# Performance work log

Measured on AMD Instinct MI355X. Metric: run time of the kernel, lower is better.

The kernel has to match this reference:

```python
import jax, jax.numpy as jnp
import numpy as np

NUM_EDGES = 800_000
NUM_VERTICES = 100_000
NNZ = 1_600_000
D_MODEL = 128


def setup_inputs() -> dict:
    key = jax.random.key(0)
    ks = jax.random.split(key, 10)
    d = D_MODEL
    return {
        "x_e": jax.random.normal(ks[0], (NUM_EDGES, d), dtype=jnp.float32),
        "h_v": jax.random.normal(ks[1], (NUM_VERTICES, d), dtype=jnp.float32),
        "c_v": jax.random.normal(ks[2], (NUM_VERTICES, d), dtype=jnp.float32),
        "W_ih": jax.random.normal(ks[3], (4 * d, d), dtype=jnp.float32) * 0.05,
        "W_hh": jax.random.normal(ks[4], (4 * d, d), dtype=jnp.float32) * 0.05,
        "b_ih": jax.random.normal(ks[5], (4 * d,), dtype=jnp.float32) * 0.05,
        "b_hh": jax.random.normal(ks[6], (4 * d,), dtype=jnp.float32) * 0.05,
        "nnz_edge_ids": jax.random.randint(ks[7], (NNZ,), 0, NUM_EDGES, dtype=jnp.int32),
        "nnz_vertex_ids": jax.random.randint(ks[8], (NNZ,), 0, NUM_VERTICES, dtype=jnp.int32),
        "v_batch": jax.random.randint(ks[9], (NUM_VERTICES,), 0, 8, dtype=jnp.int32),
    }


def reference(x_e, h_v, c_v, W_ih, W_hh, b_ih, b_hh, nnz_edge_ids, nnz_vertex_ids, v_batch):
    # msg = adj_t.T @ x_e : scatter-add edge embeddings into incident vertices
    msg = jax.ops.segment_sum(x_e[nnz_edge_ids], nnz_vertex_ids,
                              num_segments=h_v.shape[0])  # [V, d]
    # single-step LSTM update (PyTorch gate order: i, f, g, o)
    gates = msg @ W_ih.T + b_ih + h_v @ W_hh.T + b_hh  # [V, 4d]
    i, f, g, o = jnp.split(gates, 4, axis=-1)
    i = jax.nn.sigmoid(i)
    f = jax.nn.sigmoid(f)
    g = jnp.tanh(g)
    o = jax.nn.sigmoid(o)
    c_new = f * c_v + i * g
    h_new = o * jnp.tanh(c_new)
    return (h_new, c_new)
```

## Files before the change

kernel.cpp:

```cpp
#include <hip/hip_runtime.h>
#include <hip/hip_bf16.h>

#define NE 800000
#define NV 100000
#define NNZN 1600000
#define D 128
#define SLOT_CAP 64
#define SC_BLOCKS 8192

typedef short short8 __attribute__((ext_vector_type(8)));
typedef short s16x4 __attribute__((ext_vector_type(4)));
typedef float f32x4 __attribute__((ext_vector_type(4)));
typedef float f32x8 __attribute__((ext_vector_type(8)));
typedef _Float16 h8v __attribute__((ext_vector_type(8)));

__device__ __forceinline__ unsigned short f2bfu(float f) {
  union { float f; unsigned u; } x;
  x.f = f;
  unsigned u = x.u;
  u += ((u >> 16) & 1u) + 0x7FFFu;
  return (unsigned short)(u >> 16);
}

__device__ __forceinline__ float fsigmoid(float x) {
  return 1.0f / (1.0f + __expf(-x));
}
__device__ __forceinline__ float ftanh(float x) {
  return 2.0f / (1.0f + __expf(-2.0f * x)) - 1.0f;
}

__device__ __forceinline__ f32x8 h2f8(h8v h) {
  f32x8 r;
#pragma unroll
  for (int k = 0; k < 8; ++k) r[k] = (float)h[k];
  return r;
}

__global__ __launch_bounds__(256) void wconv_kernel(
    const float* __restrict__ W_ih, const float* __restrict__ W_hh,
    const float* __restrict__ b_ih, const float* __restrict__ b_hh,
    short* __restrict__ Wcat, float* __restrict__ bcomb,
    int* __restrict__ counts) {
  int idx = blockIdx.x * 256 + threadIdx.x;
  if (idx < 16384) {
    int c8 = idx;
    int pos = c8 & 63;
    int t   = (c8 >> 6) & 1;
    int g   = (c8 >> 7) & 3;
    int kk  = (c8 >> 9) & 7;
    int wid = (c8 >> 12) & 3;
    int n = g * 128 + wid * 32 + t * 16 + (pos >> 2);
    int k0 = kk * 32 + (pos & 3) * 8;
    const float* src = (k0 < 128) ? (W_ih + (size_t)n * 128 + k0)
                                  : (W_hh + (size_t)n * 128 + (k0 - 128));
    f32x4 a = *(const f32x4*)(src);
    f32x4 b = *(const f32x4*)(src + 4);
    short8 v;
    v[0] = (short)f2bfu(a[0]); v[1] = (short)f2bfu(a[1]);
    v[2] = (short)f2bfu(a[2]); v[3] = (short)f2bfu(a[3]);
    v[4] = (short)f2bfu(b[0]); v[5] = (short)f2bfu(b[1]);
    v[6] = (short)f2bfu(b[2]); v[7] = (short)f2bfu(b[3]);
    *(short8*)(Wcat + (size_t)c8 * 8) = v;
  }
  if (idx < 512) bcomb[idx] = b_ih[idx] + b_hh[idx];
  if (idx < NV) counts[idx] = 0;
}

__global__ __launch_bounds__(256) void scatcon_kernel(
    const int* __restrict__ eid, const int* __restrict__ vid,
    int* __restrict__ counts, int* __restrict__ slots,
    const float* __restrict__ x_e, _Float16* __restrict__ x_h) {
  unsigned j = blockIdx.x * 256 + threadIdx.x;
  if (j < NNZN) {
    int v = vid[j];
    int pos = atomicAdd(&counts[v], 1);
    if (pos < SLOT_CAP) slots[(size_t)v * SLOT_CAP + pos] = eid[j];
  }
  const unsigned NU = (unsigned)NE * 16u;
  for (unsigned u = j; u < NU; u += SC_BLOCKS * 256u) {
    f32x4 a = __builtin_nontemporal_load((const f32x4*)(x_e + (size_t)u * 8));
    f32x4 b = __builtin_nontemporal_load((const f32x4*)(x_e + (size_t)u * 8 + 4));
    h8v h;
    h[0] = (_Float16)a[0]; h[1] = (_Float16)a[1];
    h[2] = (_Float16)a[2]; h[3] = (_Float16)a[3];
    h[4] = (_Float16)b[0]; h[5] = (_Float16)b[1];
    h[6] = (_Float16)b[2]; h[7] = (_Float16)b[3];
    *(h8v*)(x_h + (size_t)u * 8) = h;
  }
}

__global__ __launch_bounds__(256) void scatter_direct_kernel(
    const int* __restrict__ eid, const int* __restrict__ vid,
    int* __restrict__ counts, int* __restrict__ slots) {
  int j = blockIdx.x * 256 + threadIdx.x;
  if (j < NNZN) {
    int v = vid[j];
    int pos = atomicAdd(&counts[v], 1);
    if (pos < SLOT_CAP) slots[(size_t)v * SLOT_CAP + pos] = eid[j];
  }
}

__global__ __launch_bounds__(256, 4) void gather16_kernel(
    const _Float16* __restrict__ x_h, const int* __restrict__ counts,
    const int* __restrict__ slots, char* __restrict__ msgb) {
  __shared__ int slds[4][SLOT_CAP];
  const int tid = threadIdx.x;
  const int wid = tid >> 6;
  const int lane = tid & 63;
  const int v = blockIdx.x * 4 + wid;
  const int grp = lane >> 4;
  const int p16 = lane & 15;
  int deg = counts[v];
  deg = deg > SLOT_CAP ? SLOT_CAP : deg;
  slds[wid][lane] = slots[(size_t)v * SLOT_CAP + lane];
  const int* row_ids = slds[wid];

  f32x8 A0 = {0.f,0.f,0.f,0.f,0.f,0.f,0.f,0.f};
  f32x8 A1 = A0, A2 = A0, A3 = A0;
  const f32x8 Z = A0;
  const int nfull = deg >> 5;
  const int rem = deg & 31;
#pragma unroll 1
  for (int c = 0; c < nfull; ++c) {
    int b = c * 32 + grp;
    int e0 = row_ids[b];      int e1 = row_ids[b + 4];
    int e2 = row_ids[b + 8];  int e3 = row_ids[b + 12];
    int e4 = row_ids[b + 16]; int e5 = row_ids[b + 20];
    int e6 = row_ids[b + 24]; int e7 = row_ids[b + 28];
    h8v t0 = *(const h8v*)(x_h + (size_t)e0 * D + p16 * 8);
    h8v t1 = *(const h8v*)(x_h + (size_t)e1 * D + p16 * 8);
    h8v t2 = *(const h8v*)(x_h + (size_t)e2 * D + p16 * 8);
    h8v t3 = *(const h8v*)(x_h + (size_t)e3 * D + p16 * 8);
    h8v t4 = *(const h8v*)(x_h + (size_t)e4 * D + p16 * 8);
    h8v t5 = *(const h8v*)(x_h + (size_t)e5 * D + p16 * 8);
    h8v t6 = *(const h8v*)(x_h + (size_t)e6 * D + p16 * 8);
    h8v t7 = *(const h8v*)(x_h + (size_t)e7 * D + p16 * 8);
    A0 += h2f8(t0); A1 += h2f8(t1); A2 += h2f8(t2); A3 += h2f8(t3);
    A0 += h2f8(t4); A1 += h2f8(t5); A2 += h2f8(t6); A3 += h2f8(t7);
  }
  if (rem) {
    int b = nfull * 32 + grp;
    int i0 = b,      i1 = b + 4,  i2 = b + 8,  i3 = b + 12;
    int i4 = b + 16, i5 = b + 20, i6 = b + 24, i7 = b + 28;
    int e0 = row_ids[i0 < deg ? i0 : 0];
    int e1 = row_ids[i1 < deg ? i1 : 0];
    int e2 = row_ids[i2 < deg ? i2 : 0];
    int e3 = row_ids[i3 < deg ? i3 : 0];
    int e4 = row_ids[i4 < deg ? i4 : 0];
    int e5 = row_ids[i5 < deg ? i5 : 0];
    int e6 = row_ids[i6 < deg ? i6 : 0];
    int e7 = row_ids[i7 < deg ? i7 : 0];
    h8v t0 = *(const h8v*)(x_h + (size_t)e0 * D + p16 * 8);
    h8v t1 = *(const h8v*)(x_h + (size_t)e1 * D + p16 * 8);
    h8v t2 = *(const h8v*)(x_h + (size_t)e2 * D + p16 * 8);
    h8v t3 = *(const h8v*)(x_h + (size_t)e3 * D + p16 * 8);
    h8v t4 = *(const h8v*)(x_h + (size_t)e4 * D + p16 * 8);
    h8v t5 = *(const h8v*)(x_h + (size_t)e5 * D + p16 * 8);
    h8v t6 = *(const h8v*)(x_h + (size_t)e6 * D + p16 * 8);
    h8v t7 = *(const h8v*)(x_h + (size_t)e7 * D + p16 * 8);
    A0 += (i0 < deg) ? h2f8(t0) : Z;
    A1 += (i1 < deg) ? h2f8(t1) : Z;
    A2 += (i2 < deg) ? h2f8(t2) : Z;
    A3 += (i3 < deg) ? h2f8(t3) : Z;
    A0 += (i4 < deg) ? h2f8(t4) : Z;
    A1 += (i5 < deg) ? h2f8(t5) : Z;
    A2 += (i6 < deg) ? h2f8(t6) : Z;
    A3 += (i7 < deg) ? h2f8(t7) : Z;
  }
  A0 += A1;
  A2 += A3;
  A0 += A2;
#pragma unroll
  for (int f = 0; f < 8; ++f) {
    float x = A0[f];
    x += __shfl_xor(x, 32);
    x += __shfl_xor(x, 16);
    A0[f] = x;
  }
  if (lane < 16) {
    short8 p;
#pragma unroll
    for (int f = 0; f < 8; ++f) p[f] = (short)f2bfu(A0[f]);
    *(short8*)(msgb + (size_t)v * 512 + p16 * 16) = p;
  }
}

__global__ __launch_bounds__(256, 4) void gather_kernel(
    const float* __restrict__ x_e, const int* __restrict__ counts,
    const int* __restrict__ slots, char* __restrict__ msgb) {
  __shared__ int slds[4][SLOT_CAP];
  const int tid = threadIdx.x;
  const int wid = tid >> 6;
  const int lane = tid & 63;
  const int v = blockIdx.x * 4 + wid;
  const int half = lane >> 5;
  const int pos = lane & 31;
  int deg = counts[v];
  deg = deg > SLOT_CAP ? SLOT_CAP : deg;
  slds[wid][lane] = slots[(size_t)v * SLOT_CAP + lane];
  const int* row_ids = slds[wid];

  f32x4 a0 = {0.f, 0.f, 0.f, 0.f}, a1 = a0, a2 = a0, a3 = a0;
  const int nfull = deg >> 4;
  const int rem = deg & 15;
#pragma unroll 1
  for (int c = 0; c < nfull; ++c) {
    int b = c * 16 + half;
    int e0 = row_ids[b];      int e1 = row_ids[b + 2];
    int e2 = row_ids[b + 4];  int e3 = row_ids[b + 6];
    int e4 = row_ids[b + 8];  int e5 = row_ids[b + 10];
    int e6 = row_ids[b + 12]; int e7 = row_ids[b + 14];
    a0 += *(const f32x4*)(x_e + (size_t)e0 * D + pos * 4);
    a1 += *(const f32x4*)(x_e + (size_t)e1 * D + pos * 4);
    a2 += *(const f32x4*)(x_e + (size_t)e2 * D + pos * 4);
    a3 += *(const f32x4*)(x_e + (size_t)e3 * D + pos * 4);
    a0 += *(const f32x4*)(x_e + (size_t)e4 * D + pos * 4);
    a1 += *(const f32x4*)(x_e + (size_t)e5 * D + pos * 4);
    a2 += *(const f32x4*)(x_e + (size_t)e6 * D + pos * 4);
    a3 += *(const f32x4*)(x_e + (size_t)e7 * D + pos * 4);
  }
  if (rem) {
    int b = nfull * 16 + half;
    f32x4 z = {0.f, 0.f, 0.f, 0.f};
    int i0 = b,      i1 = b + 2,  i2 = b + 4,  i3 = b + 6;
    int i4 = b + 8,  i5 = b + 10, i6 = b + 12, i7 = b + 14;
    int e0 = row_ids[i0 < deg ? i0 : 0];
    int e1 = row_ids[i1 < deg ? i1 : 0];
    int e2 = row_ids[i2 < deg ? i2 : 0];
    int e3 = row_ids[i3 < deg ? i3 : 0];
    int e4 = row_ids[i4 < deg ? i4 : 0];
    int e5 = row_ids[i5 < deg ? i5 : 0];
    int e6 = row_ids[i6 < deg ? i6 : 0];
    int e7 = row_ids[i7 < deg ? i7 : 0];
    f32x4 t0 = *(const f32x4*)(x_e + (size_t)e0 * D + pos * 4);
    f32x4 t1 = *(const f32x4*)(x_e + (size_t)e1 * D + pos * 4);
    f32x4 t2 = *(const f32x4*)(x_e + (size_t)e2 * D + pos * 4);
    f32x4 t3 = *(const f32x4*)(x_e + (size_t)e3 * D + pos * 4);
    f32x4 t4 = *(const f32x4*)(x_e + (size_t)e4 * D + pos * 4);
    f32x4 t5 = *(const f32x4*)(x_e + (size_t)e5 * D + pos * 4);
    f32x4 t6 = *(const f32x4*)(x_e + (size_t)e6 * D + pos * 4);
    f32x4 t7 = *(const f32x4*)(x_e + (size_t)e7 * D + pos * 4);
    a0 += (i0 < deg) ? t0 : z;
    a1 += (i1 < deg) ? t1 : z;
    a2 += (i2 < deg) ? t2 : z;
    a3 += (i3 < deg) ? t3 : z;
    a0 += (i4 < deg) ? t4 : z;
    a1 += (i5 < deg) ? t5 : z;
    a2 += (i6 < deg) ? t6 : z;
    a3 += (i7 < deg) ? t7 : z;
  }
  a0 += a1;
  a2 += a3;
  a0 += a2;
  f32x4 b;
  b[0] = __shfl_xor(a0[0], 32);
  b[1] = __shfl_xor(a0[1], 32);
  b[2] = __shfl_xor(a0[2], 32);
  b[3] = __shfl_xor(a0[3], 32);
  a0 += b;
  if (half == 0) {
    s16x4 p;
    p[0] = (short)f2bfu(a0[0]);
    p[1] = (short)f2bfu(a0[1]);
    p[2] = (short)f2bfu(a0[2]);
    p[3] = (short)f2bfu(a0[3]);
    *(s16x4*)(msgb + (size_t)v * 512 + pos * 8) = p;
  }
}

__global__ __launch_bounds__(256) void lstm_kernel(
    const char* __restrict__ msgb, const float* __restrict__ h_v,
    const float* __restrict__ c_v, const short* __restrict__ Wcat,
    const float* __restrict__ bcomb, float* __restrict__ out) {
  __shared__ char Atile[32 * 256 * 2];
  const int tid = threadIdx.x;
  const int vbase = blockIdx.x * 32;

#pragma unroll
  for (int i = 0; i < 4; ++i) {
    int cid = tid + i * 256;
    int row = cid >> 5;
    int c = cid & 31;
    short8 v;
    if (c < 16) {
      v = *(const short8*)(msgb + (size_t)(vbase + row) * 512 + c * 16);
    } else {
      const float* src = h_v + (size_t)(vbase + row) * D + (c - 16) * 8;
      f32x4 a = *(const f32x4*)(src);
      f32x4 b = *(const f32x4*)(src + 4);
      v[0] = (short)f2bfu(a[0]); v[1] = (short)f2bfu(a[1]);
      v[2] = (short)f2bfu(a[2]); v[3] = (short)f2bfu(a[3]);
      v[4] = (short)f2bfu(b[0]); v[5] = (short)f2bfu(b[1]);
      v[6] = (short)f2bfu(b[2]); v[7] = (short)f2bfu(b[3]);
    }
    int byteoff = (row * 512 + c * 16) ^ ((row & 7) << 4);
    *(short8*)(Atile + byteoff) = v;
  }
  __syncthreads();

  const int wid = tid >> 6;
  const int lane = tid & 63;
  const int l16 = lane & 15;
  const int lhi = lane >> 4;

  f32x4 acc[2][4][2] = {};

#pragma unroll
  for (int kk = 0; kk < 8; ++kk) {
    short8 afrag[2];
#pragma unroll
    for (int m = 0; m < 2; ++m) {
      int row = m * 16 + l16;
      int byteoff = (row * 512 + kk * 64 + lhi * 16) ^ ((row & 7) << 4);
      afrag[m] = *(const short8*)(Atile + byteoff);
    }
#pragma unroll
    for (int g = 0; g < 4; ++g) {
#pragma unroll
      for (int t = 0; t < 2; ++t) {
        size_t boff = (size_t)(wid * 64 + kk * 8 + g * 2 + t) * 1024
                    + (size_t)(l16 * 4 + lhi) * 16;
        short8 bfrag = *(const short8*)((const char*)Wcat + boff);
        acc[0][g][t] = __builtin_amdgcn_mfma_f32_16x16x32_bf16(afrag[0], bfrag, acc[0][g][t], 0, 0, 0);
        acc[1][g][t] = __builtin_amdgcn_mfma_f32_16x16x32_bf16(afrag[1], bfrag, acc[1][g][t], 0, 0, 0);
      }
    }
  }

  float* out_h = out;
  float* out_c = out + (size_t)NV * D;
#pragma unroll
  for (int m = 0; m < 2; ++m) {
#pragma unroll
    for (int t = 0; t < 2; ++t) {
      int d = wid * 32 + t * 16 + l16;
      float bi = bcomb[d];
      float bf = bcomb[128 + d];
      float bg = bcomb[256 + d];
      float bo = bcomb[384 + d];
#pragma unroll
      for (int r = 0; r < 4; ++r) {
        int v = vbase + m * 16 + lhi * 4 + r;
        float gi = acc[m][0][t][r] + bi;
        float gf = acc[m][1][t][r] + bf;
        float gg = acc[m][2][t][r] + bg;
        float go = acc[m][3][t][r] + bo;
        float ii = fsigmoid(gi);
        float ff = fsigmoid(gf);
        float g_ = ftanh(gg);
        float oo = fsigmoid(go);
        float cv = c_v[(size_t)v * D + d];
        float cn = ff * cv + ii * g_;
        float hn = oo * ftanh(cn);
        out_h[(size_t)v * D + d] = hn;
        out_c[(size_t)v * D + d] = cn;
      }
    }
  }
}

extern "C" void kernel_launch(void* const* d_in, const int* in_sizes, int n_in,
                              void* d_out, int out_size, void* d_ws, size_t ws_size,
                              hipStream_t stream) {
  const float* x_e  = (const float*)d_in[0];
  const float* h_v  = (const float*)d_in[1];
  const float* c_v  = (const float*)d_in[2];
  const float* W_ih = (const float*)d_in[3];
  const float* W_hh = (const float*)d_in[4];
  const float* b_ih = (const float*)d_in[5];
  const float* b_hh = (const float*)d_in[6];
  const int* eid    = (const int*)d_in[7];
  const int* vid    = (const int*)d_in[8];
  float* out = (float*)d_out;

  char* w = (char*)d_ws;
  short* Wcat  = (short*)w;                 w += 512 * 256 * sizeof(short);
  float* bcomb = (float*)w;                 w += 512 * sizeof(float);
  int* counts  = (int*)w;                   w += NV * sizeof(int);
  int* slots   = (int*)w;                   w += (size_t)NV * SLOT_CAP * sizeof(int);
  _Float16* x_h = (_Float16*)w;

  const size_t need = 512 * 256 * sizeof(short) + 512 * sizeof(float)
                    + (size_t)NV * sizeof(int)
                    + (size_t)NV * SLOT_CAP * sizeof(int)
                    + (size_t)NE * D * sizeof(_Float16);

  char* msgb = (char*)(out + (size_t)NV * D);

  wconv_kernel<<<512, 256, 0, stream>>>(W_ih, W_hh, b_ih, b_hh, Wcat, bcomb, counts);
  if (ws_size >= need) {
    scatcon_kernel<<<SC_BLOCKS, 256, 0, stream>>>(eid, vid, counts, slots, x_e, x_h);
    gather16_kernel<<<NV / 4, 256, 0, stream>>>(x_h, counts, slots, msgb);
  } else {
    scatter_direct_kernel<<<(NNZN + 255) / 256, 256, 0, stream>>>(eid, vid, counts, slots);
    gather_kernel<<<NV / 4, 256, 0, stream>>>(x_e, counts, slots, msgb);
  }
  lstm_kernel<<<NV / 32, 256, 0, stream>>>(msgb, h_v, c_v, Wcat, bcomb, out);
}
```

Baseline: 419.1 us.

## Convert part of edge embeddings to fp16 in output buffer and workspace, gather mixed

The scatter pass now converts only edges below a cutoff to fp16. The first 400k rows go into the output buffer, which is free until the LSTM step, and further rows go into any spare workspace. The gather kernel reads fp16 rows for low edge ids and fp32 rows straight from x_e for the rest, using a second per-vertex counter. The second list of edge ids is stored from the back of each vertex's slot array. The message buffer moves into the workspace. The aim is to get most of the halved gather traffic when the workspace cannot hold a full fp16 copy, at the cost of conversion traffic and branchier gather code.

```diff
diff --git a/kernel.cpp b/kernel.cpp
--- a/kernel.cpp
+++ b/kernel.cpp
@@ -6,6 +6,7 @@
 #define NNZN 1600000
 #define D 128
 #define SLOT_CAP 64
+#define XCUT 400000
 #define SC_BLOCKS 8192
 
 typedef short short8 __attribute__((ext_vector_type(8)));
@@ -40,7 +41,7 @@
     const float* __restrict__ W_ih, const float* __restrict__ W_hh,
     const float* __restrict__ b_ih, const float* __restrict__ b_hh,
     short* __restrict__ Wcat, float* __restrict__ bcomb,
-    int* __restrict__ counts) {
+    int* __restrict__ counts, int* __restrict__ counts2) {
   int idx = blockIdx.x * 256 + threadIdx.x;
   if (idx < 16384) {
     int c8 = idx;
@@ -63,21 +64,30 @@
     *(short8*)(Wcat + (size_t)c8 * 8) = v;
   }
   if (idx < 512) bcomb[idx] = b_ih[idx] + b_hh[idx];
-  if (idx < NV) counts[idx] = 0;
+  if (idx < NV) { counts[idx] = 0; counts2[idx] = 0; }
 }
 
 __global__ __launch_bounds__(256) void scatcon_kernel(
     const int* __restrict__ eid, const int* __restrict__ vid,
-    int* __restrict__ counts, int* __restrict__ slots,
-    const float* __restrict__ x_e, _Float16* __restrict__ x_h) {
+    int* __restrict__ counts, int* __restrict__ counts2,
+    int* __restrict__ slots, const float* __restrict__ x_e,
+    _Float16* __restrict__ xh0, _Float16* __restrict__ xh1, int ecut) {
   unsigned j = blockIdx.x * 256 + threadIdx.x;
   if (j < NNZN) {
     int v = vid[j];
-    int pos = atomicAdd(&counts[v], 1);
-    if (pos < SLOT_CAP) slots[(size_t)v * SLOT_CAP + pos] = eid[j];
-  }
-  const unsigned NU = (unsigned)NE * 16u;
+    int e = eid[j];
+    if (e < ecut) {
+      int pos = atomicAdd(&counts[v], 1);
+      if (pos < SLOT_CAP) slots[(size_t)v * SLOT_CAP + pos] = e;
+    } else {
+      int pos = atomicAdd(&counts2[v], 1);
+      if (pos < SLOT_CAP) slots[(size_t)v * SLOT_CAP + (SLOT_CAP - 1 - pos)] = e;
+    }
+  }
+  const unsigned NU = (unsigned)ecut * 16u;
   for (unsigned u = j; u < NU; u += SC_BLOCKS * 256u) {
+    unsigned row = u >> 4;
+    unsigned c8 = u & 15u;
     f32x4 a = __builtin_nontemporal_load((const f32x4*)(x_e + (size_t)u * 8));
     f32x4 b = __builtin_nontemporal_load((const f32x4*)(x_e + (size_t)u * 8 + 4));
     h8v h;
@@ -85,7 +95,9 @@
     h[2] = (_Float16)a[2]; h[3] = (_Float16)a[3];
     h[4] = (_Float16)b[0]; h[5] = (_Float16)b[1];
     h[6] = (_Float16)b[2]; h[7] = (_Float16)b[3];
-    *(h8v*)(x_h + (size_t)u * 8) = h;
+    _Float16* dst = (row < XCUT) ? (xh0 + (size_t)row * D)
+                                 : (xh1 + (size_t)(row - XCUT) * D);
+    *(h8v*)(dst + c8 * 8) = h;
   }
 }
 
@@ -100,9 +112,11 @@
   }
 }
 
-__global__ __launch_bounds__(256, 4) void gather16_kernel(
-    const _Float16* __restrict__ x_h, const int* __restrict__ counts,
-    const int* __restrict__ slots, char* __restrict__ msgb) {
+__global__ __launch_bounds__(256, 4) void gather_mixed_kernel(
+    const float* __restrict__ x_e, const _Float16* __restrict__ xh0,
+    const _Float16* __restrict__ xh1, const int* __restrict__ counts,
+    const int* __restrict__ counts2, const int* __restrict__ slots,
+    unsigned short* __restrict__ msgws) {
   __shared__ int slds[4][SLOT_CAP];
   const int tid = threadIdx.x;
   const int wid = tid >> 6;
@@ -110,63 +124,90 @@
   const int v = blockIdx.x * 4 + wid;
   const int grp = lane >> 4;
   const int p16 = lane & 15;
-  int deg = counts[v];
-  deg = deg > SLOT_CAP ? SLOT_CAP : deg;
+  int degf = counts[v];   degf = degf > SLOT_CAP ? SLOT_CAP : degf;
+  int degb = counts2[v];  degb = degb > SLOT_CAP ? SLOT_CAP : degb;
   slds[wid][lane] = slots[(size_t)v * SLOT_CAP + lane];
   const int* row_ids = slds[wid];
 
   f32x8 A0 = {0.f,0.f,0.f,0.f,0.f,0.f,0.f,0.f};
   f32x8 A1 = A0, A2 = A0, A3 = A0;
   const f32x8 Z = A0;
-  const int nfull = deg >> 5;
-  const int rem = deg & 31;
+
+  const int nfull = degf >> 5;
+  const int rem = degf & 31;
 #pragma unroll 1
   for (int c = 0; c < nfull; ++c) {
     int b = c * 32 + grp;
-    int e0 = row_ids[b];      int e1 = row_ids[b + 4];
-    int e2 = row_ids[b + 8];  int e3 = row_ids[b + 12];
-    int e4 = row_ids[b + 16]; int e5 = row_ids[b + 20];
-    int e6 = row_ids[b + 24]; int e7 = row_ids[b + 28];
-    h8v t0 = *(const h8v*)(x_h + (size_t)e0 * D + p16 * 8);
-    h8v t1 = *(const h8v*)(x_h + (size_t)e1 * D + p16 * 8);
-    h8v t2 = *(const h8v*)(x_h + (size_t)e2 * D + p16 * 8);
-    h8v t3 = *(const h8v*)(x_h + (size_t)e3 * D + p16 * 8);
-    h8v t4 = *(const h8v*)(x_h + (size_t)e4 * D + p16 * 8);
-    h8v t5 = *(const h8v*)(x_h + (size_t)e5 * D + p16 * 8);
-    h8v t6 = *(const h8v*)(x_h + (size_t)e6 * D + p16 * 8);
-    h8v t7 = *(const h8v*)(x_h + (size_t)e7 * D + p16 * 8);
+    h8v t0, t1, t2, t3, t4, t5, t6, t7;
+#pragma unroll
+    for (int k = 0; k < 8; ++k) {
+      int e = row_ids[b + 4 * k];
+      const _Float16* p = (e < XCUT) ? (xh0 + (size_t)e * D)
+                                     : (xh1 + (size_t)(e - XCUT) * D);
+      h8v t = *(const h8v*)(p + p16 * 8);
+      switch (k) {
+        case 0: t0 = t; break; case 1: t1 = t; break;
+        case 2: t2 = t; break; case 3: t3 = t; break;
+        case 4: t4 = t; break; case 5: t5 = t; break;
+        case 6: t6 = t; break; case 7: t7 = t; break;
+      }
+    }
     A0 += h2f8(t0); A1 += h2f8(t1); A2 += h2f8(t2); A3 += h2f8(t3);
     A0 += h2f8(t4); A1 += h2f8(t5); A2 += h2f8(t6); A3 += h2f8(t7);
   }
   if (rem) {
     int b = nfull * 32 + grp;
-    int i0 = b,      i1 = b + 4,  i2 = b + 8,  i3 = b + 12;
-    int i4 = b + 16, i5 = b + 20, i6 = b + 24, i7 = b + 28;
-    int e0 = row_ids[i0 < deg ? i0 : 0];
-    int e1 = row_ids[i1 < deg ? i1 : 0];
-    int e2 = row_ids[i2 < deg ? i2 : 0];
-    int e3 = row_ids[i3 < deg ? i3 : 0];
-    int e4 = row_ids[i4 < deg ? i4 : 0];
-    int e5 = row_ids[i5 < deg ? i5 : 0];
-    int e6 = row_ids[i6 < deg ? i6 : 0];
-    int e7 = row_ids[i7 < deg ? i7 : 0];
-    h8v t0 = *(const h8v*)(x_h + (size_t)e0 * D + p16 * 8);
-    h8v t1 = *(const h8v*)(x_h + (size_t)e1 * D + p16 * 8);
-    h8v t2 = *(const h8v*)(x_h + (size_t)e2 * D + p16 * 8);
-    h8v t3 = *(const h8v*)(x_h + (size_t)e3 * D + p16 * 8);
-    h8v t4 = *(const h8v*)(x_h + (size_t)e4 * D + p16 * 8);
-    h8v t5 = *(const h8v*)(x_h + (size_t)e5 * D + p16 * 8);
-    h8v t6 = *(const h8v*)(x_h + (size_t)e6 * D + p16 * 8);
-    h8v t7 = *(const h8v*)(x_h + (size_t)e7 * D + p16 * 8);
-    A0 += (i0 < deg) ? h2f8(t0) : Z;
-    A1 += (i1 < deg) ? h2f8(t1) : Z;
-    A2 += (i2 < deg) ? h2f8(t2) : Z;
-    A3 += (i3 < deg) ? h2f8(t3) : Z;
-    A0 += (i4 < deg) ? h2f8(t4) : Z;
-    A1 += (i5 < deg) ? h2f8(t5) : Z;
-    A2 += (i6 < deg) ? h2f8(t6) : Z;
-    A3 += (i7 < deg) ? h2f8(t7) : Z;
-  }
+    h8v t[8];
+    int valid[8];
+#pragma unroll
+    for (int k = 0; k < 8; ++k) {
+      int i = b + 4 * k;
+      valid[k] = (i < degf);
+      int e = row_ids[valid[k] ? i : 0];
+      const _Float16* p = (e < XCUT) ? (xh0 + (size_t)e * D)
+                                     : (xh1 + (size_t)(e - XCUT) * D);
+      t[k] = *(const h8v*)(p + p16 * 8);
+    }
+    A0 += valid[0] ? h2f8(t[0]) : Z;
+    A1 += valid[1] ? h2f8(t[1]) : Z;
+    A2 += valid[2] ? h2f8(t[2]) : Z;
+    A3 += valid[3] ? h2f8(t[3]) : Z;
+    A0 += valid[4] ? h2f8(t[4]) : Z;
+    A1 += valid[5] ? h2f8(t[5]) : Z;
+    A2 += valid[6] ? h2f8(t[6]) : Z;
+    A3 += valid[7] ? h2f8(t[7]) : Z;
+  }
+
+  if (degb) {
+    f32x4 bl0 = {0.f,0.f,0.f,0.f}, bh0 = bl0, bl1 = bl0, bh1 = bl0;
+    const f32x4 z4 = bl0;
+    const int nvb = (degb + 7) >> 3;
+#pragma unroll 1
+    for (int c = 0; c < nvb; ++c) {
+      int b = c * 8 + grp;
+      int i0 = b, i1 = b + 4;
+      int e0 = row_ids[SLOT_CAP - 1 - (i0 < degb ? i0 : 0)];
+      int e1 = row_ids[SLOT_CAP - 1 - (i1 < degb ? i1 : 0)];
+      const float* p0 = x_e + (size_t)e0 * D + p16 * 8;
+      const float* p1 = x_e + (size_t)e1 * D + p16 * 8;
+      f32x4 l0 = *(const f32x4*)(p0);
+      f32x4 h0 = *(const f32x4*)(p0 + 4);
+      f32x4 l1 = *(const f32x4*)(p1);
+      f32x4 h1 = *(const f32x4*)(p1 + 4);
+      bl0 += (i0 < degb) ? l0 : z4;
+      bh0 += (i0 < degb) ? h0 : z4;
+      bl1 += (i1 < degb) ? l1 : z4;
+      bh1 += (i1 < degb) ? h1 : z4;
+    }
+    bl0 += bl1;
+    bh0 += bh1;
+#pragma unroll
+    for (int k = 0; k < 4; ++k) {
+      A0[k] += bl0[k];
+      A0[4 + k] += bh0[k];
+    }
+  }
+
   A0 += A1;
   A2 += A3;
   A0 += A2;
@@ -181,7 +222,7 @@
     short8 p;
 #pragma unroll
     for (int f = 0; f < 8; ++f) p[f] = (short)f2bfu(A0[f]);
-    *(short8*)(msgb + (size_t)v * 512 + p16 * 16) = p;
+    *(short8*)(msgws + (size_t)v * D + p16 * 8) = p;
   }
 }
 
@@ -269,9 +310,10 @@
 }
 
 __global__ __launch_bounds__(256) void lstm_kernel(
-    const char* __restrict__ msgb, const float* __restrict__ h_v,
-    const float* __restrict__ c_v, const short* __restrict__ Wcat,
-    const float* __restrict__ bcomb, float* __restrict__ out) {
+    const char* __restrict__ msgb, int msg_stride,
+    const float* __restrict__ h_v, const float* __restrict__ c_v,
+    const short* __restrict__ Wcat, const float* __restrict__ bcomb,
+    float* __restrict__ out) {
   __shared__ char Atile[32 * 256 * 2];
   const int tid = threadIdx.x;
   const int vbase = blockIdx.x * 32;
@@ -283,7 +325,7 @@
     int c = cid & 31;
     short8 v;
     if (c < 16) {
-      v = *(const short8*)(msgb + (size_t)(vbase + row) * 512 + c * 16);
+      v = *(const short8*)(msgb + (size_t)(vbase + row) * msg_stride + c * 16);
     } else {
       const float* src = h_v + (size_t)(vbase + row) * D + (c - 16) * 8;
       f32x4 a = *(const f32x4*)(src);
@@ -374,26 +416,41 @@
   float* out = (float*)d_out;
 
   char* w = (char*)d_ws;
-  short* Wcat  = (short*)w;                 w += 512 * 256 * sizeof(short);
-  float* bcomb = (float*)w;                 w += 512 * sizeof(float);
-  int* counts  = (int*)w;                   w += NV * sizeof(int);
-  int* slots   = (int*)w;                   w += (size_t)NV * SLOT_CAP * sizeof(int);
-  _Float16* x_h = (_Float16*)w;
-
-  const size_t need = 512 * 256 * sizeof(short) + 512 * sizeof(float)
-                    + (size_t)NV * sizeof(int)
-                    + (size_t)NV * SLOT_CAP * sizeof(int)
-                    + (size_t)NE * D * sizeof(_Float16);
-
-  char* msgb = (char*)(out + (size_t)NV * D);
-
-  wconv_kernel<<<512, 256, 0, stream>>>(W_ih, W_hh, b_ih, b_hh, Wcat, bcomb, counts);
-  if (ws_size >= need) {
-    scatcon_kernel<<<SC_BLOCKS, 256, 0, stream>>>(eid, vid, counts, slots, x_e, x_h);
-    gather16_kernel<<<NV / 4, 256, 0, stream>>>(x_h, counts, slots, msgb);
+  short* Wcat   = (short*)w;                w += 512 * 256 * sizeof(short);
+  float* bcomb  = (float*)w;                w += 512 * sizeof(float);
+  int* counts   = (int*)w;                  w += NV * sizeof(int);
+  int* counts2  = (int*)w;                  w += NV * sizeof(int);
+  int* slots    = (int*)w;                  w += (size_t)NV * SLOT_CAP * sizeof(int);
+  unsigned short* msgws = (unsigned short*)w;  w += (size_t)NV * D * sizeof(unsigned short);
+  _Float16* xh1 = (_Float16*)w;
+
+  const size_t base_end = 512 * 256 * sizeof(short) + 512 * sizeof(float)
+                        + 2 * (size_t)NV * sizeof(int)
+                        + (size_t)NV * SLOT_CAP * sizeof(int)
+                        + (size_t)NV * D * sizeof(unsigned short);
+
+  if (ws_size >= base_end) {
+    _Float16* xh0 = (_Float16*)out;
+    size_t spare = ws_size - base_end;
+    size_t extra = spare / 256;
+    if (extra > (size_t)(NE - XCUT)) extra = NE - XCUT;
+    int ecut = XCUT + (int)(extra & ~(size_t)31);
+    wconv_kernel<<<512, 256, 0, stream>>>(W_ih, W_hh, b_ih, b_hh, Wcat, bcomb,
+                                          counts, counts2);
+    scatcon_kernel<<<SC_BLOCKS, 256, 0, stream>>>(eid, vid, counts, counts2,
+                                                  slots, x_e, xh0, xh1, ecut);
+    gather_mixed_kernel<<<NV / 4, 256, 0, stream>>>(x_e, xh0, xh1, counts,
+                                                    counts2, slots, msgws);
+    lstm_kernel<<<NV / 32, 256, 0, stream>>>((const char*)msgws, 256, h_v, c_v,
+                                             Wcat, bcomb, out);
   } else {
-    scatter_direct_kernel<<<(NNZN + 255) / 256, 256, 0, stream>>>(eid, vid, counts, slots);
+    char* msgb = (char*)(out + (size_t)NV * D);
+    wconv_kernel<<<512, 256, 0, stream>>>(W_ih, W_hh, b_ih, b_hh, Wcat, bcomb,
+                                          counts, counts2);
+    scatter_direct_kernel<<<(NNZN + 255) / 256, 256, 0, stream>>>(eid, vid,
+                                                                  counts, slots);
     gather_kernel<<<NV / 4, 256, 0, stream>>>(x_e, counts, slots, msgb);
-  }
-  lstm_kernel<<<NV / 32, 256, 0, stream>>>(msgb, h_v, c_v, Wcat, bcomb, out);
-}
+    lstm_kernel<<<NV / 32, 256, 0, stream>>>(msgb, 512, h_v, c_v, Wcat, bcomb,
+                                             out);
+  }
+}
```

Measured after the change: 405.4 us. 1.03x faster.
